# Optimization experiments

Measured on AMD Instinct MI355X. Metric: run time of the kernel, lower is better.

The kernel has to match this reference:

```python
import jax, jax.numpy as jnp
import numpy as np

EPS = 1e-5
SCALES = jnp.array([7.0, 7.0, 4.0], dtype=jnp.float32)  # (W, H, T) per source buffer
OUT_T, OUT_H, OUT_W = 3, 5, 5


def _roi_align3d(feat, start, end):
    """feat: [C,T,H,W]; start/end: [3] = (x, y, t). One sample per bin (bin center),
    trilinear interpolation, out-of-bounds -> 0 (standard ROIAlign convention)."""
    C, T, H, W = feat.shape
    dt = feat.dtype

    def centers(s, e, n):
        b = (e - s) / n
        return s + (jnp.arange(n, dtype=dt) + 0.5) * b

    xc = centers(start[0], end[0], OUT_W)  # [Wo]
    yc = centers(start[1], end[1], OUT_H)  # [Ho]
    tc = centers(start[2], end[2], OUT_T)  # [To]

    def prep(c, size):
        valid = ((c >= -1.0) & (c <= size)).astype(dt)
        c = jnp.clip(c, 0.0, size - 1)
        lo = jnp.floor(c).astype(jnp.int32)
        hi = jnp.minimum(lo + 1, size - 1)
        f = c - lo.astype(dt)
        return (lo, hi), ((1.0 - f) * valid, f * valid)

    ti, tw = prep(tc, T)
    yi, yw = prep(yc, H)
    xi, xw = prep(xc, W)

    out = jnp.zeros((C, OUT_T, OUT_H, OUT_W), dtype=dt)
    for a in range(2):
        for b in range(2):
            for c in range(2):
                g = feat[:, ti[a][:, None, None], yi[b][None, :, None], xi[c][None, None, :]]
                w = tw[a][:, None, None] * yw[b][None, :, None] * xw[c][None, None, :]
                out = out + g * w
    return out


def setup_inputs() -> dict:
    key = jax.random.key(0)
    k0, k1, k2 = jax.random.split(key, 3)
    B, C, T, H, W = 128, 1024, 4, 7, 7
    R = 256
    x = jax.random.normal(k0, (B, C, T, H, W), jnp.float32)
    w1 = jax.random.normal(k1, (R, C), jnp.float32) / np.sqrt(C).astype(np.float32)
    w2 = jax.random.normal(k2, (6, R), jnp.float32) / np.sqrt(R).astype(np.float32)
    return dict(
        x=x, w1=w1,
        g1=jnp.ones((R,), jnp.float32), b1=jnp.zeros((R,), jnp.float32),
        m1=jnp.zeros((R,), jnp.float32), v1=jnp.ones((R,), jnp.float32),
        w2=w2,
        g2=jnp.ones((6,), jnp.float32), b2=jnp.zeros((6,), jnp.float32),
        m2=jnp.zeros((6,), jnp.float32), v2=jnp.ones((6,), jnp.float32),
    )


def reference(x, w1, g1, b1, m1, v1, w2, g2, b2, m2, v2):
    # roi head: conv1x1x1 -> BN(eval) -> HSwish -> global avgpool -> conv1x1x1 -> BN(eval)
    h = jnp.einsum('bcthw,rc->brthw', x, w1)
    s1 = (g1 / jnp.sqrt(v1 + EPS))
    h = (h - m1[None, :, None, None, None]) * s1[None, :, None, None, None] + b1[None, :, None, None, None]
    h = h * jnp.clip(h + 3.0, 0.0, 6.0) * (1.0 / 6.0)  # HSwish
    h = h.mean(axis=(2, 3, 4))                          # AvgPool3d over full (T,H,W) -> [B,R]
    logits = h @ w2.T
    logits = (logits - m2) * (g2 / jnp.sqrt(v2 + EPS)) + b2  # [B,6]
    raw = jax.nn.sigmoid(logits)
    roi_start = 0.5 * raw[:, :3] * SCALES              # (x1,y1,t1)
    roi_end = (1.0 - 0.5 * raw[:, 3:]) * SCALES        # (x2,y2,t2)
    return jax.vmap(_roi_align3d)(x, roi_start, roi_end)  # [B,C,3,5,5]
```

## Files before the change

### kernel.cpp

```cpp
#include <hip/hip_runtime.h>

typedef __bf16 bf16x8 __attribute__((ext_vector_type(8)));
typedef __bf16 bf16x4 __attribute__((ext_vector_type(4)));
typedef float f32x4 __attribute__((ext_vector_type(4)));

#define EPS_F 1e-5f

__global__ __launch_bounds__(512) void k_gemm_pool(
    const float* __restrict__ x,
    const float* __restrict__ w1,
    const float* __restrict__ g1,
    const float* __restrict__ b1,
    const float* __restrict__ m1,
    const float* __restrict__ v1,
    float* __restrict__ pooled_part)
{
    constexpr int LDK = 40;
    __shared__ __bf16 Alds[112 * LDK];
    __shared__ __bf16 Blds[256 * LDK];
    __shared__ float pool_lds[2][256];

    const int b   = blockIdx.x;
    const int mc  = blockIdx.y;
    const int tid = threadIdx.x;
    const int wave = tid >> 6, lane = tid & 63;
    const int wm = wave >> 2, wn = wave & 3;
    const int q  = lane >> 4, ln = lane & 15;
    const int nm = (wm == 0) ? 4 : 3;

    f32x4 acc[4][4];
#pragma unroll
    for (int i = 0; i < 4; i++)
#pragma unroll
        for (int j = 0; j < 4; j++) acc[i][j] = (f32x4){0.f, 0.f, 0.f, 0.f};

    const int c4  = tid & 7;
    const int p4  = tid >> 3;
    const bool a_act = (p4 < 28);
    const int  pg    = mc * 28 + p4;
    const bool a_val = a_act && (pg < 49);
    const float* xb = x + (size_t)b * (1024 * 196) + pg * 4;

    const int rB = tid & 255, kh = tid >> 8;
    const float* wrow = w1 + (size_t)rB * 1024 + kh * 16;

    float  fA[4][4];
    float4 fB[4];

    auto loadA = [&](int kc) {
        if (a_val) {
#pragma unroll
            for (int i = 0; i < 4; i++) {
                const float4 f = *(const float4*)(xb + (size_t)(kc + c4 * 4 + i) * 196);
                fA[i][0] = f.x; fA[i][1] = f.y; fA[i][2] = f.z; fA[i][3] = f.w;
            }
        } else {
#pragma unroll
            for (int i = 0; i < 4; i++)
#pragma unroll
                for (int j = 0; j < 4; j++) fA[i][j] = 0.f;
        }
    };
    auto loadB = [&](int kc) {
#pragma unroll
        for (int j = 0; j < 4; j++)
            fB[j] = *(const float4*)(wrow + kc + j * 4);
    };

    loadB(0);
    if (a_act) loadA(0);

    for (int kc = 0; kc < 1024; kc += 32) {
        __syncthreads();
        {
            bf16x8 lo = {(__bf16)fB[0].x, (__bf16)fB[0].y, (__bf16)fB[0].z, (__bf16)fB[0].w,
                         (__bf16)fB[1].x, (__bf16)fB[1].y, (__bf16)fB[1].z, (__bf16)fB[1].w};
            bf16x8 hi = {(__bf16)fB[2].x, (__bf16)fB[2].y, (__bf16)fB[2].z, (__bf16)fB[2].w,
                         (__bf16)fB[3].x, (__bf16)fB[3].y, (__bf16)fB[3].z, (__bf16)fB[3].w};
            *(bf16x8*)&Blds[rB * LDK + kh * 16]     = lo;
            *(bf16x8*)&Blds[rB * LDK + kh * 16 + 8] = hi;
        }
        if (a_act) {
#pragma unroll
            for (int j = 0; j < 4; j++) {
                bf16x4 o = {(__bf16)fA[0][j], (__bf16)fA[1][j],
                            (__bf16)fA[2][j], (__bf16)fA[3][j]};
                *(bf16x4*)&Alds[(p4 * 4 + j) * LDK + c4 * 4] = o;
            }
        }
        if (kc + 32 < 1024) {
            loadB(kc + 32);
            if (a_act) loadA(kc + 32);
        }
        __syncthreads();
        bf16x8 bfr[4];
#pragma unroll
        for (int ni = 0; ni < 4; ni++)
            bfr[ni] = *(const bf16x8*)&Blds[((wn * 4 + ni) * 16 + ln) * LDK + q * 8];
#pragma unroll
        for (int mi = 0; mi < 4; mi++) {
            if (mi < nm) {
                const bf16x8 af = *(const bf16x8*)&Alds[((wm * 4 + mi) * 16 + ln) * LDK + q * 8];
#pragma unroll
                for (int ni = 0; ni < 4; ni++)
                    acc[mi][ni] = __builtin_amdgcn_mfma_f32_16x16x32_bf16(af, bfr[ni], acc[mi][ni], 0, 0, 0);
            }
        }
    }

    float psum[4] = {0.f, 0.f, 0.f, 0.f};
#pragma unroll
    for (int ni = 0; ni < 4; ni++) {
        const int r = (wn * 4 + ni) * 16 + ln;
        const float s1 = g1[r] * rsqrtf(v1[r] + EPS_F);
        const float mu = m1[r];
        const float be = b1[r];
#pragma unroll
        for (int mi = 0; mi < 4; mi++) {
            if (mi < nm) {
#pragma unroll
                for (int i = 0; i < 4; i++) {
                    const int m = mc * 112 + (wm * 4 + mi) * 16 + q * 4 + i;
                    if (m < 196) {
                        float v = acc[mi][ni][i];
                        v = (v - mu) * s1 + be;
                        const float g = fminf(fmaxf(v + 3.f, 0.f), 6.f);
                        psum[ni] += v * g * (1.f / 6.f);
                    }
                }
            }
        }
    }
#pragma unroll
    for (int ni = 0; ni < 4; ni++) {
        psum[ni] += __shfl_xor(psum[ni], 16, 64);
        psum[ni] += __shfl_xor(psum[ni], 32, 64);
    }
    if (lane < 16) {
#pragma unroll
        for (int ni = 0; ni < 4; ni++)
            pool_lds[wm][(wn * 4 + ni) * 16 + lane] = psum[ni];
    }
    __syncthreads();
    if (tid < 256)
        pooled_part[(size_t)mc * (128 * 256) + b * 256 + tid] =
            (pool_lds[0][tid] + pool_lds[1][tid]) * (1.f / 196.f);
}

__global__ __launch_bounds__(64) void k_logits(
    const float* __restrict__ pooled_part,
    const float* __restrict__ w2,
    const float* __restrict__ g2,
    const float* __restrict__ b2,
    const float* __restrict__ m2,
    const float* __restrict__ v2,
    float* __restrict__ roi)
{
    const int b = blockIdx.x, t = threadIdx.x;
    const float4 pa = ((const float4*)(pooled_part + b * 256))[t];
    const float4 pb = ((const float4*)(pooled_part + 128 * 256 + b * 256))[t];
    float4 p4;
    p4.x = pa.x + pb.x; p4.y = pa.y + pb.y;
    p4.z = pa.z + pb.z; p4.w = pa.w + pb.w;
    float part[6];
#pragma unroll
    for (int j = 0; j < 6; j++) {
        const float4 w = *(const float4*)(w2 + j * 256 + t * 4);
        part[j] = p4.x * w.x + p4.y * w.y + p4.z * w.z + p4.w * w.w;
    }
#pragma unroll
    for (int j = 0; j < 6; j++)
#pragma unroll
        for (int off = 32; off >= 1; off >>= 1)
            part[j] += __shfl_xor(part[j], off, 64);
    if (t == 0) {
        const float SC[3] = {7.f, 7.f, 4.f};
        float raw[6];
#pragma unroll
        for (int j = 0; j < 6; j++) {
            float l = part[j];
            const float s = g2[j] * rsqrtf(v2[j] + EPS_F);
            l = (l - m2[j]) * s + b2[j];
            raw[j] = 1.f / (1.f + expf(-l));
        }
#pragma unroll
        for (int d = 0; d < 3; d++) {
            roi[b * 6 + d]     = 0.5f * raw[d] * SC[d];
            roi[b * 6 + 3 + d] = (1.f - 0.5f * raw[3 + d]) * SC[d];
        }
    }
}

__device__ __forceinline__ void prep1(float s, float e, int n, int size, int i,
                                      int& lo, int& hi, float& w0, float& w1)
{
    const float bsz = (e - s) / (float)n;
    float c = s + ((float)i + 0.5f) * bsz;
    const float valid = (c >= -1.f && c <= (float)size) ? 1.f : 0.f;
    c = fminf(fmaxf(c, 0.f), (float)(size - 1));
    lo = (int)floorf(c);
    hi = min(lo + 1, size - 1);
    const float f = c - (float)lo;
    w0 = (1.f - f) * valid;
    w1 = f * valid;
}

__global__ __launch_bounds__(256) void k_roi(
    const float* __restrict__ x,
    const float* __restrict__ roi,
    float* __restrict__ out)
{
    __shared__ float xs[32 * 200];
    __shared__ int   soff[8][80];
    __shared__ float swt[8][80];

    const int b = blockIdx.x, c0 = blockIdx.y * 32;
    const int tid = threadIdx.x;

    const float* xb = x + ((size_t)b * 1024 + c0) * 196;
#pragma unroll
    for (int k = 0; k < 7; k++) {
        const int i4 = tid + k * 256;
        if (i4 < 1568) {
            const int c = i4 / 49, pq = i4 % 49;
            const float4 v = *(const float4*)(xb + c * 196 + pq * 4);
            *(float4*)&xs[c * 200 + pq * 4] = v;
        }
    }
    if (tid < 75) {
        const int po = tid;
        const int to = po / 25, rem = po % 25, yo = rem / 5, xo = rem % 5;
        const float sx = roi[b * 6 + 0], ex = roi[b * 6 + 3];
        const float sy = roi[b * 6 + 1], ey = roi[b * 6 + 4];
        const float st = roi[b * 6 + 2], et = roi[b * 6 + 5];
        int tl, th, yl, yh, xl, xh;
        float tw0, tw1, yw0, yw1, xw0, xw1;
        prep1(st, et, 3, 4, to, tl, th, tw0, tw1);
        prep1(sy, ey, 5, 7, yo, yl, yh, yw0, yw1);
        prep1(sx, ex, 5, 7, xo, xl, xh, xw0, xw1);
#pragma unroll
        for (int s = 0; s < 8; s++) {
            const int   ti = (s & 4) ? th : tl;
            const int   yi = (s & 2) ? yh : yl;
            const int   xi = (s & 1) ? xh : xl;
            const float w = ((s & 4) ? tw1 : tw0) *
                            ((s & 2) ? yw1 : yw0) *
                            ((s & 1) ? xw1 : xw0);
            soff[s][po] = ti * 49 + yi * 7 + xi;
            swt[s][po]  = w;
        }
    }
    __syncthreads();

    const size_t obase = ((size_t)b * 1024 + c0) * 75;
#pragma unroll
    for (int k = 0; k < 10; k++) {
        const int e = tid + k * 256;
        if (e < 2400) {
            const int c = e / 75, po = e % 75;
            const float* row = &xs[c * 200];
            float v = 0.f;
#pragma unroll
            for (int s = 0; s < 8; s++)
                v += swt[s][po] * row[soff[s][po]];
            out[obase + e] = v;
        }
    }
}

extern "C" void kernel_launch(void* const* d_in, const int* in_sizes, int n_in,
                              void* d_out, int out_size, void* d_ws, size_t ws_size,
                              hipStream_t stream)
{
    const float* x  = (const float*)d_in[0];
    const float* w1 = (const float*)d_in[1];
    const float* g1 = (const float*)d_in[2];
    const float* b1 = (const float*)d_in[3];
    const float* m1 = (const float*)d_in[4];
    const float* v1 = (const float*)d_in[5];
    const float* w2 = (const float*)d_in[6];
    const float* g2 = (const float*)d_in[7];
    const float* b2 = (const float*)d_in[8];
    const float* m2 = (const float*)d_in[9];
    const float* v2 = (const float*)d_in[10];

    float* pooled_part = (float*)d_ws;
    float* roi         = pooled_part + 2 * 128 * 256;
    float* out         = (float*)d_out;

    k_gemm_pool<<<dim3(128, 2), 512, 0, stream>>>(x, w1, g1, b1, m1, v1, pooled_part);
    k_logits<<<128, 64, 0, stream>>>(pooled_part, w2, g2, b2, m2, v2, roi);
    k_roi<<<dim3(128, 32), 256, 0, stream>>>(x, roi, out);
}
```

Measured before the change: 241.6 us.

## Load weight fragments directly to registers and double-buffer A tile in LDS

Each wave now loads its B (w1) fragments straight from global memory into registers in MFMA operand layout, with no staging through shared memory. The A tile is double-buffered in LDS with a two-stage register prefetch, so each k-step needs one barrier instead of two. This removes LDS traffic and a sync per iteration. In exchange, w1 reads are redundant across the two wm wave rows and use narrower, less coalesced global loads, and register pressure goes up.

```diff
diff --git a/kernel.cpp b/kernel.cpp
--- a/kernel.cpp
+++ b/kernel.cpp
@@ -16,8 +16,7 @@
     float* __restrict__ pooled_part)
 {
     constexpr int LDK = 40;
-    __shared__ __bf16 Alds[112 * LDK];
-    __shared__ __bf16 Blds[256 * LDK];
+    __shared__ __bf16 Alds[2][112 * LDK];
     __shared__ float pool_lds[2][256];
 
     const int b   = blockIdx.x;
@@ -41,12 +40,7 @@
     const bool a_val = a_act && (pg < 49);
     const float* xb = x + (size_t)b * (1024 * 196) + pg * 4;
 
-    const int rB = tid & 255, kh = tid >> 8;
-    const float* wrow = w1 + (size_t)rB * 1024 + kh * 16;
-
-    float  fA[4][4];
-    float4 fB[4];
-
+    float fA[4][4];
     auto loadA = [&](int kc) {
         if (a_val) {
 #pragma unroll
@@ -61,51 +55,57 @@
                 for (int j = 0; j < 4; j++) fA[i][j] = 0.f;
         }
     };
+    auto storeA = [&](int buf) {
+#pragma unroll
+        for (int j = 0; j < 4; j++) {
+            bf16x4 o = {(__bf16)fA[0][j], (__bf16)fA[1][j],
+                        (__bf16)fA[2][j], (__bf16)fA[3][j]};
+            *(bf16x4*)&Alds[buf][(p4 * 4 + j) * LDK + c4 * 4] = o;
+        }
+    };
+
+    const float* wBr = w1 + (size_t)(wn * 64 + ln) * 1024 + q * 8;
+    float4 fB[4][2];
     auto loadB = [&](int kc) {
 #pragma unroll
-        for (int j = 0; j < 4; j++)
-            fB[j] = *(const float4*)(wrow + kc + j * 4);
+        for (int ni = 0; ni < 4; ni++) {
+            fB[ni][0] = *(const float4*)(wBr + ni * 16384 + kc);
+            fB[ni][1] = *(const float4*)(wBr + ni * 16384 + kc + 4);
+        }
     };
 
+    if (a_act) { loadA(0); storeA(0); loadA(32); }
     loadB(0);
-    if (a_act) loadA(0);
-
-    for (int kc = 0; kc < 1024; kc += 32) {
-        __syncthreads();
-        {
-            bf16x8 lo = {(__bf16)fB[0].x, (__bf16)fB[0].y, (__bf16)fB[0].z, (__bf16)fB[0].w,
-                         (__bf16)fB[1].x, (__bf16)fB[1].y, (__bf16)fB[1].z, (__bf16)fB[1].w};
-            bf16x8 hi = {(__bf16)fB[2].x, (__bf16)fB[2].y, (__bf16)fB[2].z, (__bf16)fB[2].w,
-                         (__bf16)fB[3].x, (__bf16)fB[3].y, (__bf16)fB[3].z, (__bf16)fB[3].w};
-            *(bf16x8*)&Blds[rB * LDK + kh * 16]     = lo;
-            *(bf16x8*)&Blds[rB * LDK + kh * 16 + 8] = hi;
-        }
-        if (a_act) {
-#pragma unroll
-            for (int j = 0; j < 4; j++) {
-                bf16x4 o = {(__bf16)fA[0][j], (__bf16)fA[1][j],
-                            (__bf16)fA[2][j], (__bf16)fA[3][j]};
-                *(bf16x4*)&Alds[(p4 * 4 + j) * LDK + c4 * 4] = o;
-            }
-        }
-        if (kc + 32 < 1024) {
-            loadB(kc + 32);
-            if (a_act) loadA(kc + 32);
-        }
-        __syncthreads();
+    asm volatile("s_waitcnt lgkmcnt(0)" ::: "memory");
+    __builtin_amdgcn_s_barrier();
+
+    for (int kc = 0, t = 0; kc < 1024; kc += 32, ++t) {
+        const int cur = t & 1;
         bf16x8 bfr[4];
 #pragma unroll
         for (int ni = 0; ni < 4; ni++)
-            bfr[ni] = *(const bf16x8*)&Blds[((wn * 4 + ni) * 16 + ln) * LDK + q * 8];
+            bfr[ni] = (bf16x8){(__bf16)fB[ni][0].x, (__bf16)fB[ni][0].y,
+                               (__bf16)fB[ni][0].z, (__bf16)fB[ni][0].w,
+                               (__bf16)fB[ni][1].x, (__bf16)fB[ni][1].y,
+                               (__bf16)fB[ni][1].z, (__bf16)fB[ni][1].w};
+        if (kc + 32 < 1024) loadB(kc + 32);
+        if (a_act && kc + 32 < 1024) {
+            storeA(cur ^ 1);
+            if (kc + 64 < 1024) loadA(kc + 64);
+        }
 #pragma unroll
         for (int mi = 0; mi < 4; mi++) {
             if (mi < nm) {
-                const bf16x8 af = *(const bf16x8*)&Alds[((wm * 4 + mi) * 16 + ln) * LDK + q * 8];
+                const bf16x8 af =
+                    *(const bf16x8*)&Alds[cur][((wm * 4 + mi) * 16 + ln) * LDK + q * 8];
 #pragma unroll
                 for (int ni = 0; ni < 4; ni++)
-                    acc[mi][ni] = __builtin_amdgcn_mfma_f32_16x16x32_bf16(af, bfr[ni], acc[mi][ni], 0, 0, 0);
+                    acc[mi][ni] = __builtin_amdgcn_mfma_f32_16x16x32_bf16(
+                        af, bfr[ni], acc[mi][ni], 0, 0, 0);
             }
         }
+        asm volatile("s_waitcnt lgkmcnt(0)" ::: "memory");
+        __builtin_amdgcn_s_barrier();
     }
 
     float psum[4] = {0.f, 0.f, 0.f, 0.f};
```

New measurement: 245.8 us. About the same (+1.7%).
